# Optimization experiments

Hardware: AMD Instinct MI355X
Metric: run time of the kernel (lower is better)

The kernel has to match this reference:

```python
import jax, jax.numpy as jnp
import numpy as np

N_ENT = 50000
N_REL = 16
D_E = 64
D_R = 64
D_OUT = 32
N_EDGE = 1000000


def setup_inputs() -> dict:
    key = jax.random.key(0)
    ks = jax.random.split(key, 8)
    # 0.1 scale keeps tanh / softmax in a realistic (non-saturated) range,
    # mimicking trained embedding magnitudes.
    entity_table = jax.random.normal(ks[0], (N_ENT, D_E), dtype=jnp.float32) * 0.1
    relation_table = jax.random.normal(ks[1], (N_REL, D_R), dtype=jnp.float32) * 0.1
    W_R = jax.random.normal(ks[2], (N_REL, D_E, D_R), dtype=jnp.float32) * (1.0 / np.sqrt(D_E))
    W1 = jax.random.normal(ks[3], (D_E, D_OUT), dtype=jnp.float32) * (1.0 / np.sqrt(D_E))
    b1 = jnp.zeros((D_OUT,), dtype=jnp.float32)
    W2 = jax.random.normal(ks[4], (D_E, D_OUT), dtype=jnp.float32) * (1.0 / np.sqrt(D_E))
    b2 = jnp.zeros((D_OUT,), dtype=jnp.float32)
    src = jax.random.randint(ks[5], (N_EDGE,), 0, N_ENT, dtype=jnp.int32)
    dst = jax.random.randint(ks[6], (N_EDGE,), 0, N_ENT, dtype=jnp.int32)
    etype = jax.random.randint(ks[7], (N_EDGE,), 0, N_REL, dtype=jnp.int32)
    return {"entity_table": entity_table, "relation_table": relation_table,
            "W_R": W_R, "W1": W1, "b1": b1, "W2": W2, "b2": b2,
            "src": src, "dst": dst, "etype": etype}


def reference(entity_table, relation_table, W_R, W1, b1, W2, b2, src, dst, etype):
    """KGAT calc_att (per-relation edge attention + edge softmax) followed by
    one bi-interaction Aggregator layer (dropout = identity, eval mode)."""
    n_nodes = entity_table.shape[0]
    # Per-relation projection of all node embeddings (grouped GEMM form of the
    # per-relation loop in compute_attention): [R, N, d_r]
    proj = jnp.einsum('nd,rde->rne', entity_table, W_R)
    r_mul_h = proj[etype, src]            # [E, d_r]  h W_r per edge
    r_mul_t = proj[etype, dst]            # [E, d_r]  t W_r per edge
    r_e = relation_table[etype]           # [E, d_r]
    # att = (h W_r) . tanh(t W_r + r)
    att = jnp.sum(r_mul_h * jnp.tanh(r_mul_t + r_e), axis=-1)  # [E]
    # edge softmax grouped by destination node
    att_max = jax.ops.segment_max(att, dst, num_segments=n_nodes)     # [N]
    ex = jnp.exp(att - att_max[dst])
    denom = jax.ops.segment_sum(ex, dst, num_segments=n_nodes)        # [N]
    a = ex / denom[dst]                                               # [E]
    # u_mul_e + sum: N_h[v] = sum_{(u->v)} a_e * node[u]
    msg = a[:, None] * entity_table[src]                              # [E, d]
    N_h = jax.ops.segment_sum(msg, dst, num_segments=n_nodes)         # [N, d]
    node = entity_table
    # bi-interaction aggregator (LeakyReLU slope 0.01, torch default)
    out1 = jax.nn.leaky_relu((node + N_h) @ W1 + b1)
    out2 = jax.nn.leaky_relu((node * N_h) @ W2 + b2)
    return out1 + out2
```

## Files before the change

kernel.cpp:

```cpp
#include <hip/hip_runtime.h>
#include <math.h>

#define NREL 16
#define DE 64
#define DOUT 32
#define NPART 16
#define TQ 392

typedef __attribute__((ext_vector_type(8))) short bf16x8;
typedef __attribute__((ext_vector_type(16))) float f32x16;
typedef __attribute__((ext_vector_type(2))) float f32x2;

__device__ __forceinline__ short f2bf(float f) {
    unsigned u = __builtin_bit_cast(unsigned, f);
    unsigned r = (u + 0x7FFFu + ((u >> 16) & 1u)) >> 16;
    return (short)r;
}
__device__ __forceinline__ float bf2f(short s) {
    unsigned u = ((unsigned)(unsigned short)s) << 16;
    return __builtin_bit_cast(float, u);
}
__device__ __forceinline__ unsigned char f2fp8(float f) {
    int p = __builtin_amdgcn_cvt_pk_fp8_f32(f, f, 0, false);
    return (unsigned char)(p & 0xff);
}
__device__ __forceinline__ float tanh_fast(float x) {
    float e = __expf(2.0f * x);
    return fmaf(-2.0f, __builtin_amdgcn_rcpf(e + 1.0f), 1.0f);
}

__global__ __launch_bounds__(256) void prep_kernel(const float* __restrict__ ent,
                                                   short* __restrict__ entbf, int eTot,
                                                   const float* __restrict__ WR,
                                                   short* __restrict__ Wbf,
                                                   short* __restrict__ WTbf,
                                                   const int* __restrict__ dst,
                                                   int* __restrict__ counts,
                                                   int E, int psz,
                                                   int eB, int wB) {
    int b = blockIdx.x;
    if (b < eB) {
        int i = b * 256 + threadIdx.x;
        if (i < eTot) entbf[i] = f2bf(ent[i]);
    } else if (b < eB + wB) {
        int i = (b - eB) * 256 + threadIdx.x;
        int r = i >> 12, k = (i >> 6) & 63, j = i & 63;
        short w = f2bf(WR[i]);
        Wbf[i] = w;
        WTbf[(r << 12) + (j << 6) + k] = w;
    } else {
        int hb = b - eB - wB;
        int part = hb & (NPART - 1);
        int i = (hb / NPART) * 256 + threadIdx.x;
        if (i < E) {
            int d = dst[i];
            if (d >= part * psz && d < (part + 1) * psz)
                atomicAdd(&counts[d], 1);
        }
    }
}

__global__ __launch_bounds__(256) void blocksum_kernel(const int* __restrict__ counts,
                                                       int* __restrict__ blockSums, int n) {
    __shared__ int wsum[4];
    int i = blockIdx.x * 256 + threadIdx.x;
    int v = (i < n) ? counts[i] : 0;
#pragma unroll
    for (int off = 1; off < 64; off <<= 1) v += __shfl_xor(v, off);
    if ((threadIdx.x & 63) == 0) wsum[threadIdx.x >> 6] = v;
    __syncthreads();
    if (threadIdx.x == 0)
        blockSums[blockIdx.x] = wsum[0] + wsum[1] + wsum[2] + wsum[3];
}

__global__ __launch_bounds__(1024) void blockscan_kernel(int* __restrict__ blockSums, int nb) {
    __shared__ int lds[1024];
    int t = threadIdx.x;
    int v = (t < nb) ? blockSums[t] : 0;
    lds[t] = v;
    __syncthreads();
    for (int off = 1; off < 1024; off <<= 1) {
        int u = (t >= off) ? lds[t - off] : 0;
        __syncthreads();
        lds[t] += u;
        __syncthreads();
    }
    if (t < nb) blockSums[t] = (t == 0) ? 0 : lds[t - 1];
}

__global__ __launch_bounds__(256) void scanout_kernel(const int* __restrict__ counts,
                                                      const int* __restrict__ blockSums,
                                                      int* __restrict__ offsets,
                                                      int* __restrict__ cursor, int n) {
    __shared__ int wsum[4];
    int t = threadIdx.x;
    int i = blockIdx.x * 256 + t;
    int lane = t & 63;
    int w = t >> 6;
    int v = (i < n) ? counts[i] : 0;
    int incl = v;
#pragma unroll
    for (int off = 1; off < 64; off <<= 1) {
        int u = __shfl_up(incl, off);
        if (lane >= off) incl += u;
    }
    if (lane == 63) wsum[w] = incl;
    __syncthreads();
    int woff = 0;
#pragma unroll
    for (int j = 0; j < 4; ++j) if (j < w) woff += wsum[j];
    int excl = incl - v + woff + blockSums[blockIdx.x];
    if (i < n) { offsets[i] = excl; cursor[i] = excl; }
    if (i == n - 1) offsets[n] = excl + v;
}

__global__ __launch_bounds__(256) void scatter_kernel(const int* __restrict__ dst,
                                                      const int* __restrict__ src,
                                                      const int* __restrict__ etype,
                                                      int* __restrict__ cursor,
                                                      int* __restrict__ pks,
                                                      int E, int psz) {
    int part = blockIdx.x & (NPART - 1);
    int i = (blockIdx.x / NPART) * 256 + threadIdx.x;
    if (i < E) {
        int d = dst[i];
        if (d >= part * psz && d < (part + 1) * psz) {
            int pos = atomicAdd(&cursor[d], 1);
            pks[pos] = (src[i] << 4) | etype[i];
        }
    }
}

__global__ __launch_bounds__(256) void projq_kernel(const short* __restrict__ entbf,
                                                    const float* __restrict__ rel,
                                                    const short* __restrict__ Wbf,
                                                    const short* __restrict__ WTbf,
                                                    unsigned char* __restrict__ Qf8,
                                                    int N) {
    __shared__ short Tl[4 * 2048];
    int lane = threadIdx.x & 63;
    int wid = threadIdx.x >> 6;
    int lin = blockIdx.x;
    int r = lin / TQ;
    int tq = lin - r * TQ;
    int m0 = (tq * 4 + wid) * 32;
    if (m0 >= N) return;
    int hi = lane >> 5;
    int lo = lane & 31;

    int arow = m0 + lo;
    if (arow >= N) arow = N - 1;
    const short* ap = entbf + ((size_t)arow << 6) + hi * 8;
    bf16x8 A[4];
#pragma unroll
    for (int kk = 0; kk < 4; ++kk) A[kk] = *(const bf16x8*)(ap + kk * 16);

    short* tb = Tl + wid * 2048;
    const short* wtb = WTbf + ((size_t)r << 12);
    const short* wb  = Wbf  + ((size_t)r << 12);

    f32x16 acc0 = {}, acc1 = {};
#pragma unroll
    for (int kk = 0; kk < 4; ++kk) {
        bf16x8 b0 = *(const bf16x8*)(wtb + lo * DE + kk * 16 + hi * 8);
        bf16x8 b1 = *(const bf16x8*)(wtb + (lo + 32) * DE + kk * 16 + hi * 8);
        acc0 = __builtin_amdgcn_mfma_f32_32x32x16_bf16(A[kk], b0, acc0, 0, 0, 0);
        acc1 = __builtin_amdgcn_mfma_f32_32x32x16_bf16(A[kk], b1, acc1, 0, 0, 0);
    }
    float rv0 = rel[r * DE + lo];
    float rv1 = rel[r * DE + 32 + lo];
#pragma unroll
    for (int i = 0; i < 16; ++i) {
        int row = (i & 3) + 8 * (i >> 2) + 4 * hi;
        int sw = (row & 7) << 3;
        tb[(row * DE + lo) ^ sw] = f2bf(tanh_fast(acc0[i] + rv0));
        tb[(row * DE + 32 + lo) ^ sw] = f2bf(tanh_fast(acc1[i] + rv1));
    }
    bf16x8 A2[4];
#pragma unroll
    for (int kk = 0; kk < 4; ++kk)
        A2[kk] = *(const bf16x8*)(tb + ((lo * DE + kk * 16 + hi * 8) ^ ((lo & 7) << 3)));

    f32x16 q0 = {}, q1 = {};
#pragma unroll
    for (int kk = 0; kk < 4; ++kk) {
        bf16x8 b0 = *(const bf16x8*)(wb + lo * DE + kk * 16 + hi * 8);
        bf16x8 b1 = *(const bf16x8*)(wb + (lo + 32) * DE + kk * 16 + hi * 8);
        q0 = __builtin_amdgcn_mfma_f32_32x32x16_bf16(A2[kk], b0, q0, 0, 0, 0);
        q1 = __builtin_amdgcn_mfma_f32_32x32x16_bf16(A2[kk], b1, q1, 0, 0, 0);
    }
    unsigned char* tb8 = (unsigned char*)tb;
#pragma unroll
    for (int i = 0; i < 16; ++i) {
        int row = (i & 3) + 8 * (i >> 2) + 4 * hi;
        tb8[row * DE + lo] = f2fp8(q0[i]);
        tb8[row * DE + 32 + lo] = f2fp8(q1[i]);
    }
#pragma unroll
    for (int p = 0; p < 4; ++p) {
        int row = p * 8 + (lane >> 3);
        int node = m0 + row;
        unsigned long long vq = *(const unsigned long long*)(tb8 + row * DE + (lane & 7) * 8);
        if (node < N)
            __builtin_nontemporal_store(vq,
                (unsigned long long*)(Qf8 + (((size_t)r * N + node) << 6) + (lane & 7) * 8));
    }
}

__global__ __launch_bounds__(256) void agg_kernel(const float* __restrict__ ent,
                                                  const short* __restrict__ entbf,
                                                  const unsigned char* __restrict__ Qf8,
                                                  const int* __restrict__ offsets,
                                                  const int* __restrict__ pks,
                                                  const float* __restrict__ W1,
                                                  const float* __restrict__ b1,
                                                  const float* __restrict__ W2,
                                                  const float* __restrict__ b2,
                                                  float* __restrict__ out, int n) {
    __shared__ float xl[4][128];
    int lane = threadIdx.x & 63;
    int wid = threadIdx.x >> 6;
    int v = (blockIdx.x << 2) + wid;
    if (v >= n) return;
    int o0 = offsets[v], o1 = offsets[v + 1];
    int g = lane >> 3, gl = lane & 7;
    const unsigned char* qbase = Qf8 + ((size_t)v << 6) + gl * 8;

    float m = -INFINITY, l = 0.f;
    float acc[8];
#pragma unroll
    for (int j = 0; j < 8; ++j) acc[j] = 0.f;

    int k = o0 + g;
    bool val = k < o1;
    bf16x8 xv = {};
    uint2 qv = {};
    if (val) {
        int pk = pks[k];
        xv = *(const bf16x8*)(entbf + ((size_t)(pk >> 4) << 6) + gl * 8);
        qv = *(const uint2*)(qbase + (((size_t)(pk & 15) * (size_t)n) << 6));
    }
    int kn = k + 8;
    bool valn = kn < o1;
    int pkn = valn ? pks[kn] : 0;

    int iters = (o1 - o0 + 7) >> 3;
    for (int it = 0; it < iters; ++it) {
        bf16x8 xn = {};
        uint2 qn = {};
        if (valn) {
            xn = *(const bf16x8*)(entbf + ((size_t)(pkn >> 4) << 6) + gl * 8);
            qn = *(const uint2*)(qbase + (((size_t)(pkn & 15) * (size_t)n) << 6));
        }
        int kn2 = kn + 8;
        bool valn2 = kn2 < o1;
        int pkn2 = valn2 ? pks[kn2] : 0;

        f32x2 qa = __builtin_amdgcn_cvt_pk_f32_fp8(qv.x, false);
        f32x2 qb = __builtin_amdgcn_cvt_pk_f32_fp8(qv.x, true);
        f32x2 qc = __builtin_amdgcn_cvt_pk_f32_fp8(qv.y, false);
        f32x2 qd = __builtin_amdgcn_cvt_pk_f32_fp8(qv.y, true);
        float qf[8] = {qa[0], qa[1], qb[0], qb[1], qc[0], qc[1], qd[0], qd[1]};
        float xf[8];
        float d = 0.f;
#pragma unroll
        for (int j = 0; j < 8; ++j) {
            xf[j] = bf2f(xv[j]);
            d = fmaf(xf[j], qf[j], d);
        }
        d += __shfl_xor(d, 1);
        d += __shfl_xor(d, 2);
        d += __shfl_xor(d, 4);
        float p = val ? d : -INFINITY;
        float nm = fmaxf(m, p);
        float sc, pe;
        if (nm == -INFINITY) { sc = 0.f; pe = 0.f; }
        else { sc = __expf(m - nm); pe = __expf(p - nm); }
        l = l * sc + pe;
#pragma unroll
        for (int j = 0; j < 8; ++j) acc[j] = fmaf(acc[j], sc, pe * xf[j]);
        m = nm;
        val = valn; xv = xn; qv = qn;
        kn = kn2; valn = valn2; pkn = pkn2;
    }
#pragma unroll
    for (int off = 8; off < 64; off <<= 1) {
        float mo = __shfl_xor(m, off);
        float lo2 = __shfl_xor(l, off);
        float nm = fmaxf(m, mo);
        float s1 = (nm == -INFINITY) ? 0.f : __expf(m - nm);
        float s2 = (nm == -INFINITY) ? 0.f : __expf(mo - nm);
        l = l * s1 + lo2 * s2;
#pragma unroll
        for (int j = 0; j < 8; ++j) {
            float ao = __shfl_xor(acc[j], off);
            acc[j] = acc[j] * s1 + ao * s2;
        }
        m = nm;
    }
    float* xw = &xl[wid][0];
    float invl = (l > 0.f) ? (1.0f / l) : 0.f;
    if (g == 0) {
#pragma unroll
        for (int j = 0; j < 8; ++j) xw[gl * 8 + j] = acc[j] * invl;
    }
    float node = ent[((size_t)v << 6) + lane];
    float Nh = xw[lane];
    float x1 = node + Nh;
    float x2 = node * Nh;
    xw[lane] = x1;
    xw[64 + lane] = x2;
    int j = lane & 31;
    const float* __restrict__ Wsel = (lane < 32) ? W1 : W2;
    float bias = (lane < 32) ? b1[j] : b2[j];
    const float* xb = xw + ((lane < 32) ? 0 : 64);
    float o = 0.f;
#pragma unroll 8
    for (int kk = 0; kk < DE; ++kk)
        o = fmaf(xb[kk], Wsel[kk * DOUT + j], o);
    o += bias;
    float lr = (o > 0.f) ? o : 0.01f * o;
    float other = __shfl_xor(lr, 32);
    if (lane < 32) out[(size_t)v * DOUT + lane] = lr + other;
}

extern "C" void kernel_launch(void* const* d_in, const int* in_sizes, int n_in,
                              void* d_out, int out_size, void* d_ws, size_t ws_size,
                              hipStream_t stream) {
    const float* ent = (const float*)d_in[0];
    const float* rel = (const float*)d_in[1];
    const float* WR  = (const float*)d_in[2];
    const float* W1  = (const float*)d_in[3];
    const float* b1  = (const float*)d_in[4];
    const float* W2  = (const float*)d_in[5];
    const float* b2  = (const float*)d_in[6];
    const int* src   = (const int*)d_in[7];
    const int* dst   = (const int*)d_in[8];
    const int* ety   = (const int*)d_in[9];
    float* out       = (float*)d_out;

    const int E = in_sizes[7];
    const int N = in_sizes[0] / DE;
    const int NB = (N + 255) / 256;
    const int psz = (N + NPART - 1) / NPART;
    const int chunks = (E + 255) / 256;

    size_t qBytes  = (size_t)N * NREL * DE;
    size_t eElems  = (size_t)N * DE;
    size_t wElems  = (size_t)NREL * DE * DE;

    char* ws = (char*)d_ws;
    unsigned char* Qf8 = (unsigned char*)ws;
    short* entbf = (short*)(ws + qBytes);
    short* Wbf   = entbf + eElems;
    short* WTbf  = Wbf + wElems;
    int* counts  = (int*)(WTbf + wElems);
    int* offsets = counts + N;
    int* cursor  = offsets + N + 1;
    int* pks     = cursor + N;
    int* bsums   = pks + E;
    size_t need  = (size_t)((char*)(bsums + NB) - ws);
    if (ws_size < need) return;

    const int eB = (int)((eElems + 255) / 256);
    const int wB = (int)(wElems / 256);

    hipMemsetAsync(counts, 0, (size_t)N * 4, stream);
    prep_kernel<<<eB + wB + chunks * NPART, 256, 0, stream>>>(
        ent, entbf, (int)eElems, WR, Wbf, WTbf, dst, counts, E, psz, eB, wB);
    blocksum_kernel<<<NB, 256, 0, stream>>>(counts, bsums, N);
    blockscan_kernel<<<1, 1024, 0, stream>>>(bsums, NB);
    scanout_kernel<<<NB, 256, 0, stream>>>(counts, bsums, offsets, cursor, N);
    scatter_kernel<<<chunks * NPART, 256, 0, stream>>>(dst, src, ety, cursor, pks, E, psz);
    projq_kernel<<<TQ * NREL, 256, 0, stream>>>(entbf, rel, Wbf, WTbf, Qf8, N);
    agg_kernel<<<(N + 3) / 4, 256, 0, stream>>>(ent, entbf, Qf8, offsets, pks,
                                                W1, b1, W2, b2, out, N);
}
```

Baseline: 237.4 us.

## Store per-relation projections and compute tanh per destination in aggregation

Previously the projection kernel computed Q = tanh(x W_r + r) W_r^T per node and relation, a second GEMM, so the score was x_src · Q_dst. Now it stores only P = x W_r in fp8. The aggregation kernel builds tanh(P_dst + r) for all 16 relations of its destination node in shared memory and dots it with the gathered P_src row. This removes the second MFMA pass and the Wbf copy. In exchange each destination does 16×64 tanh evaluations, uses 8KB more LDS per wave, and gathers fp8 source projections instead of reusing bf16 entity rows for the dot product. Accuracy may change because P_src is now quantized to fp8.

```diff
diff --git a/kernel.cpp b/kernel.cpp
--- a/kernel.cpp
+++ b/kernel.cpp
@@ -24,6 +24,11 @@
     int p = __builtin_amdgcn_cvt_pk_fp8_f32(f, f, 0, false);
     return (unsigned char)(p & 0xff);
 }
+__device__ __forceinline__ unsigned cvt_pk_bf16(float lo, float hi) {
+    unsigned r;
+    asm("v_cvt_pk_bf16_f32 %0, %1, %2" : "=v"(r) : "v"(lo), "v"(hi));
+    return r;
+}
 __device__ __forceinline__ float tanh_fast(float x) {
     float e = __expf(2.0f * x);
     return fmaf(-2.0f, __builtin_amdgcn_rcpf(e + 1.0f), 1.0f);
@@ -32,7 +37,6 @@
 __global__ __launch_bounds__(256) void prep_kernel(const float* __restrict__ ent,
                                                    short* __restrict__ entbf, int eTot,
                                                    const float* __restrict__ WR,
-                                                   short* __restrict__ Wbf,
                                                    short* __restrict__ WTbf,
                                                    const int* __restrict__ dst,
                                                    int* __restrict__ counts,
@@ -45,9 +49,7 @@
     } else if (b < eB + wB) {
         int i = (b - eB) * 256 + threadIdx.x;
         int r = i >> 12, k = (i >> 6) & 63, j = i & 63;
-        short w = f2bf(WR[i]);
-        Wbf[i] = w;
-        WTbf[(r << 12) + (j << 6) + k] = w;
+        WTbf[(r << 12) + (j << 6) + k] = f2bf(WR[i]);
     } else {
         int hb = b - eB - wB;
         int part = hb & (NPART - 1);
@@ -131,13 +133,11 @@
     }
 }
 
-__global__ __launch_bounds__(256) void projq_kernel(const short* __restrict__ entbf,
-                                                    const float* __restrict__ rel,
-                                                    const short* __restrict__ Wbf,
+__global__ __launch_bounds__(256) void projp_kernel(const short* __restrict__ entbf,
                                                     const short* __restrict__ WTbf,
-                                                    unsigned char* __restrict__ Qf8,
+                                                    unsigned char* __restrict__ Pf8,
                                                     int N) {
-    __shared__ short Tl[4 * 2048];
+    __shared__ short Tl[4 * 1024];
     int lane = threadIdx.x & 63;
     int wid = threadIdx.x >> 6;
     int lin = blockIdx.x;
@@ -155,9 +155,7 @@
 #pragma unroll
     for (int kk = 0; kk < 4; ++kk) A[kk] = *(const bf16x8*)(ap + kk * 16);
 
-    short* tb = Tl + wid * 2048;
     const short* wtb = WTbf + ((size_t)r << 12);
-    const short* wb  = Wbf  + ((size_t)r << 12);
 
     f32x16 acc0 = {}, acc1 = {};
 #pragma unroll
@@ -167,34 +165,12 @@
         acc0 = __builtin_amdgcn_mfma_f32_32x32x16_bf16(A[kk], b0, acc0, 0, 0, 0);
         acc1 = __builtin_amdgcn_mfma_f32_32x32x16_bf16(A[kk], b1, acc1, 0, 0, 0);
     }
-    float rv0 = rel[r * DE + lo];
-    float rv1 = rel[r * DE + 32 + lo];
+    unsigned char* tb8 = (unsigned char*)(Tl + wid * 1024);
 #pragma unroll
     for (int i = 0; i < 16; ++i) {
         int row = (i & 3) + 8 * (i >> 2) + 4 * hi;
-        int sw = (row & 7) << 3;
-        tb[(row * DE + lo) ^ sw] = f2bf(tanh_fast(acc0[i] + rv0));
-        tb[(row * DE + 32 + lo) ^ sw] = f2bf(tanh_fast(acc1[i] + rv1));
-    }
-    bf16x8 A2[4];
-#pragma unroll
-    for (int kk = 0; kk < 4; ++kk)
-        A2[kk] = *(const bf16x8*)(tb + ((lo * DE + kk * 16 + hi * 8) ^ ((lo & 7) << 3)));
-
-    f32x16 q0 = {}, q1 = {};
-#pragma unroll
-    for (int kk = 0; kk < 4; ++kk) {
-        bf16x8 b0 = *(const bf16x8*)(wb + lo * DE + kk * 16 + hi * 8);
-        bf16x8 b1 = *(const bf16x8*)(wb + (lo + 32) * DE + kk * 16 + hi * 8);
-        q0 = __builtin_amdgcn_mfma_f32_32x32x16_bf16(A2[kk], b0, q0, 0, 0, 0);
-        q1 = __builtin_amdgcn_mfma_f32_32x32x16_bf16(A2[kk], b1, q1, 0, 0, 0);
-    }
-    unsigned char* tb8 = (unsigned char*)tb;
-#pragma unroll
-    for (int i = 0; i < 16; ++i) {
-        int row = (i & 3) + 8 * (i >> 2) + 4 * hi;
-        tb8[row * DE + lo] = f2fp8(q0[i]);
-        tb8[row * DE + 32 + lo] = f2fp8(q1[i]);
+        tb8[row * DE + lo] = f2fp8(acc0[i]);
+        tb8[row * DE + 32 + lo] = f2fp8(acc1[i]);
     }
 #pragma unroll
     for (int p = 0; p < 4; ++p) {
@@ -203,13 +179,14 @@
         unsigned long long vq = *(const unsigned long long*)(tb8 + row * DE + (lane & 7) * 8);
         if (node < N)
             __builtin_nontemporal_store(vq,
-                (unsigned long long*)(Qf8 + (((size_t)r * N + node) << 6) + (lane & 7) * 8));
+                (unsigned long long*)(Pf8 + (((size_t)r * N + node) << 6) + (lane & 7) * 8));
     }
 }
 
 __global__ __launch_bounds__(256) void agg_kernel(const float* __restrict__ ent,
                                                   const short* __restrict__ entbf,
-                                                  const unsigned char* __restrict__ Qf8,
+                                                  const unsigned char* __restrict__ Pf8,
+                                                  const float* __restrict__ rel,
                                                   const int* __restrict__ offsets,
                                                   const int* __restrict__ pks,
                                                   const float* __restrict__ W1,
@@ -218,13 +195,28 @@
                                                   const float* __restrict__ b2,
                                                   float* __restrict__ out, int n) {
     __shared__ float xl[4][128];
+    __shared__ short tl[4][NREL * DE];
     int lane = threadIdx.x & 63;
     int wid = threadIdx.x >> 6;
     int v = (blockIdx.x << 2) + wid;
     if (v >= n) return;
     int o0 = offsets[v], o1 = offsets[v + 1];
     int g = lane >> 3, gl = lane & 7;
-    const unsigned char* qbase = Qf8 + ((size_t)v << 6) + gl * 8;
+
+    short* tw = &tl[wid][0];
+    const unsigned char* pv = Pf8 + ((size_t)v << 6);
+#pragma unroll
+    for (int pass = 0; pass < 4; ++pass) {
+        int r = pass * 4 + (lane >> 4);
+        int j4 = (lane & 15) * 4;
+        unsigned pj = *(const unsigned*)(pv + (((size_t)r * (unsigned)n) << 6) + j4);
+        f32x2 pa = __builtin_amdgcn_cvt_pk_f32_fp8(pj, false);
+        f32x2 pb = __builtin_amdgcn_cvt_pk_f32_fp8(pj, true);
+        float4 rv = *(const float4*)(rel + r * DE + j4);
+        unsigned lo32 = cvt_pk_bf16(tanh_fast(pa[0] + rv.x), tanh_fast(pa[1] + rv.y));
+        unsigned hi32 = cvt_pk_bf16(tanh_fast(pb[0] + rv.z), tanh_fast(pb[1] + rv.w));
+        *(uint2*)(&tw[r * DE + j4]) = make_uint2(lo32, hi32);
+    }
 
     float m = -INFINITY, l = 0.f;
     float acc[8];
@@ -234,11 +226,14 @@
     int k = o0 + g;
     bool val = k < o1;
     bf16x8 xv = {};
-    uint2 qv = {};
+    uint2 hv = {};
+    int rcur = 0;
     if (val) {
         int pk = pks[k];
+        rcur = pk & 15;
+        unsigned idx = (unsigned)rcur * (unsigned)n + (unsigned)(pk >> 4);
         xv = *(const bf16x8*)(entbf + ((size_t)(pk >> 4) << 6) + gl * 8);
-        qv = *(const uint2*)(qbase + (((size_t)(pk & 15) * (size_t)n) << 6));
+        hv = *(const uint2*)(Pf8 + ((size_t)idx << 6) + gl * 8);
     }
     int kn = k + 8;
     bool valn = kn < o1;
@@ -247,26 +242,29 @@
     int iters = (o1 - o0 + 7) >> 3;
     for (int it = 0; it < iters; ++it) {
         bf16x8 xn = {};
-        uint2 qn = {};
+        uint2 hn = {};
+        int rnext = pkn & 15;
         if (valn) {
+            unsigned idx = (unsigned)rnext * (unsigned)n + (unsigned)(pkn >> 4);
             xn = *(const bf16x8*)(entbf + ((size_t)(pkn >> 4) << 6) + gl * 8);
-            qn = *(const uint2*)(qbase + (((size_t)(pkn & 15) * (size_t)n) << 6));
+            hn = *(const uint2*)(Pf8 + ((size_t)idx << 6) + gl * 8);
         }
         int kn2 = kn + 8;
         bool valn2 = kn2 < o1;
         int pkn2 = valn2 ? pks[kn2] : 0;
 
-        f32x2 qa = __builtin_amdgcn_cvt_pk_f32_fp8(qv.x, false);
-        f32x2 qb = __builtin_amdgcn_cvt_pk_f32_fp8(qv.x, true);
-        f32x2 qc = __builtin_amdgcn_cvt_pk_f32_fp8(qv.y, false);
-        f32x2 qd = __builtin_amdgcn_cvt_pk_f32_fp8(qv.y, true);
-        float qf[8] = {qa[0], qa[1], qb[0], qb[1], qc[0], qc[1], qd[0], qd[1]};
+        bf16x8 tt = *(const bf16x8*)(&tw[rcur * DE + gl * 8]);
+        f32x2 ha = __builtin_amdgcn_cvt_pk_f32_fp8(hv.x, false);
+        f32x2 hb = __builtin_amdgcn_cvt_pk_f32_fp8(hv.x, true);
+        f32x2 hc = __builtin_amdgcn_cvt_pk_f32_fp8(hv.y, false);
+        f32x2 hd = __builtin_amdgcn_cvt_pk_f32_fp8(hv.y, true);
+        float hf[8] = {ha[0], ha[1], hb[0], hb[1], hc[0], hc[1], hd[0], hd[1]};
         float xf[8];
         float d = 0.f;
 #pragma unroll
         for (int j = 0; j < 8; ++j) {
             xf[j] = bf2f(xv[j]);
-            d = fmaf(xf[j], qf[j], d);
+            d = fmaf(hf[j], bf2f(tt[j]), d);
         }
         d += __shfl_xor(d, 1);
         d += __shfl_xor(d, 2);
@@ -280,7 +278,7 @@
 #pragma unroll
         for (int j = 0; j < 8; ++j) acc[j] = fmaf(acc[j], sc, pe * xf[j]);
         m = nm;
-        val = valn; xv = xn; qv = qn;
+        val = valn; xv = xn; hv = hn; rcur = rnext;
         kn = kn2; valn = valn2; pkn = pkn2;
     }
 #pragma unroll
@@ -345,15 +343,14 @@
     const int psz = (N + NPART - 1) / NPART;
     const int chunks = (E + 255) / 256;
 
-    size_t qBytes  = (size_t)N * NREL * DE;
+    size_t pBytes  = (size_t)N * NREL * DE;
     size_t eElems  = (size_t)N * DE;
     size_t wElems  = (size_t)NREL * DE * DE;
 
     char* ws = (char*)d_ws;
-    unsigned char* Qf8 = (unsigned char*)ws;
-    short* entbf = (short*)(ws + qBytes);
-    short* Wbf   = entbf + eElems;
-    short* WTbf  = Wbf + wElems;
+    unsigned char* Pf8 = (unsigned char*)ws;
+    short* entbf = (short*)(ws + pBytes);
+    short* WTbf  = entbf + eElems;
     int* counts  = (int*)(WTbf + wElems);
     int* offsets = counts + N;
     int* cursor  = offsets + N + 1;
@@ -367,12 +364,12 @@
 
     hipMemsetAsync(counts, 0, (size_t)N * 4, stream);
     prep_kernel<<<eB + wB + chunks * NPART, 256, 0, stream>>>(
-        ent, entbf, (int)eElems, WR, Wbf, WTbf, dst, counts, E, psz, eB, wB);
+        ent, entbf, (int)eElems, WR, WTbf, dst, counts, E, psz, eB, wB);
     blocksum_kernel<<<NB, 256, 0, stream>>>(counts, bsums, N);
     blockscan_kernel<<<1, 1024, 0, stream>>>(bsums, NB);
     scanout_kernel<<<NB, 256, 0, stream>>>(counts, bsums, offsets, cursor, N);
     scatter_kernel<<<chunks * NPART, 256, 0, stream>>>(dst, src, ety, cursor, pks, E, psz);
-    projq_kernel<<<TQ * NREL, 256, 0, stream>>>(entbf, rel, Wbf, WTbf, Qf8, N);
-    agg_kernel<<<(N + 3) / 4, 256, 0, stream>>>(ent, entbf, Qf8, offsets, pks,
+    projp_kernel<<<TQ * NREL, 256, 0, stream>>>(entbf, WTbf, Pf8, N);
+    agg_kernel<<<(N + 3) / 4, 256, 0, stream>>>(ent, entbf, Pf8, rel, offsets, pks,
                                                 W1, b1, W2, b2, out, N);
 }
```

Measured after the change: 219.0 us. 1.08x faster.
